# Kernel tuning notes

Measured on AMD Instinct MI355X. Metric: run time of the kernel, lower is better.

## Reference

```python
import jax, jax.numpy as jnp
import numpy as np

N, E, G, H, IN = 200000, 400000, 64, 128, 5
LN_EPS = 1e-5


def setup_inputs() -> dict:
    key = jax.random.key(0)
    ks = jax.random.split(key, 32)
    d = {}
    d["x"] = jax.random.normal(ks[0], (N, IN), jnp.float32)
    d["edge_index"] = jax.random.randint(ks[1], (2, E), 0, N, dtype=jnp.int32)
    d["edge_attr"] = jax.random.normal(ks[2], (E, 1), jnp.float32)
    d["batch"] = jnp.sort(jax.random.randint(ks[3], (N,), 0, G, dtype=jnp.int32))
    dims = [IN, H, H]
    i = 4
    names = [("ew", "eb", "w1_", "b1_", "w2_", "b2_", "g", "bt")]
    for l, din in enumerate(dims):
        d[f"ew{l}"] = jax.random.normal(ks[i], (1, din), jnp.float32); i += 1
        d[f"eb{l}"] = jnp.zeros((din,), jnp.float32)
        d[f"w1_{l}"] = jax.random.normal(ks[i], (din, H), jnp.float32) / np.sqrt(din); i += 1
        d[f"b1_{l}"] = jnp.zeros((H,), jnp.float32)
        d[f"w2_{l}"] = jax.random.normal(ks[i], (H, H), jnp.float32) / np.sqrt(H); i += 1
        d[f"b2_{l}"] = jnp.zeros((H,), jnp.float32)
        d[f"g{l}"] = jnp.ones((H,), jnp.float32)
        d[f"bt{l}"] = jnp.zeros((H,), jnp.float32)
    return d


def _gine_layer(x, src, dst, edge_attr, ew, eb, w1, b1, w2, b2, g, bt):
    # edge encoder: Linear(1, din)
    e = edge_attr @ ew + eb                       # [E, din]
    # GINEConv message: ReLU(x_j + e), aggregated (sum) at destination
    m = jax.nn.relu(x[src] + e)                   # [E, din]
    aggr = jax.ops.segment_sum(m, dst, num_segments=N)  # [N, din]
    h = x + aggr                                  # (1 + eps)*x with eps=0
    # GIN MLP: Linear -> ReLU -> Linear
    h = jax.nn.relu(h @ w1 + b1) @ w2 + b2        # [N, H]
    # LayerNorm
    mu = jnp.mean(h, axis=-1, keepdims=True)
    var = jnp.mean((h - mu) ** 2, axis=-1, keepdims=True)
    h = (h - mu) * jax.lax.rsqrt(var + LN_EPS) * g + bt
    return jax.nn.relu(h)


def reference(x, edge_index, edge_attr, batch,
              ew0, eb0, w1_0, b1_0, w2_0, b2_0, g0, bt0,
              ew1, eb1, w1_1, b1_1, w2_1, b2_1, g1, bt1,
              ew2, eb2, w1_2, b1_2, w2_2, b2_2, g2, bt2):
    src, dst = edge_index[0], edge_index[1]
    x = _gine_layer(x, src, dst, edge_attr, ew0, eb0, w1_0, b1_0, w2_0, b2_0, g0, bt0)
    x = _gine_layer(x, src, dst, edge_attr, ew1, eb1, w1_1, b1_1, w2_1, b2_1, g1, bt1)
    x = _gine_layer(x, src, dst, edge_attr, ew2, eb2, w1_2, b1_2, w2_2, b2_2, g2, bt2)
    # global pooling per graph
    add_pool = jax.ops.segment_sum(x, batch, num_segments=G)           # [G, H]
    counts = jax.ops.segment_sum(jnp.ones((N,), x.dtype), batch, num_segments=G)
    mean_pool = add_pool / jnp.maximum(counts, 1.0)[:, None]           # [G, H]
    return jnp.concatenate([mean_pool, add_pool], axis=1)              # [G, 2H]
```

## Files before the change

kernel.cpp:

```cpp
#include <hip/hip_runtime.h>

#define N_NODES 200000
#define N_EDGES 400000
#define N_GRAPHS 64
#define HDIM 128
#define INDIM 5
#define LN_EPS 1e-5f
#define LDA 138

typedef __attribute__((ext_vector_type(8))) short short8;
typedef __attribute__((ext_vector_type(4))) float f32x4;

__device__ __forceinline__ unsigned short to_bf(float v) {
    unsigned u = __builtin_bit_cast(unsigned, v);
    return (unsigned short)((u + 0x7FFFu + ((u >> 16) & 1u)) >> 16);
}
__device__ __forceinline__ float bf_lo(unsigned w) { return __builtin_bit_cast(float, w << 16); }
__device__ __forceinline__ float bf_hi(unsigned w) { return __builtin_bit_cast(float, w & 0xFFFF0000u); }
__device__ __forceinline__ float bf2f(unsigned short h) { return __builtin_bit_cast(float, (unsigned)h << 16); }


__global__ void hist_kernel(const int* __restrict__ ei, int* __restrict__ deg) {
    int e = blockIdx.x * blockDim.x + threadIdx.x;
    if (e < N_EDGES) atomicAdd(&deg[ei[N_EDGES + e]], 1);
}

#define SCAN_CHUNK 1024
#define SCAN_BLOCKS ((N_NODES + SCAN_CHUNK - 1) / SCAN_CHUNK)

__global__ __launch_bounds__(256) void scan_phaseA(const int* __restrict__ deg, int* __restrict__ bsums) {
    __shared__ int red[256];
    int t = threadIdx.x;
    int base = blockIdx.x * SCAN_CHUNK + t * 4;
    int s = 0;
#pragma unroll
    for (int k = 0; k < 4; ++k) {
        int i = base + k;
        s += (i < N_NODES) ? deg[i] : 0;
    }
    red[t] = s;
    __syncthreads();
    for (int off = 128; off; off >>= 1) {
        if (t < off) red[t] += red[t + off];
        __syncthreads();
    }
    if (t == 0) bsums[blockIdx.x] = red[0];
}

__global__ __launch_bounds__(256) void scan_phaseB(int* __restrict__ bsums, int* __restrict__ row_ptr) {
    __shared__ int s[256];
    int t = threadIdx.x;
    int v = (t < SCAN_BLOCKS) ? bsums[t] : 0;
    s[t] = v;
    __syncthreads();
    for (int off = 1; off < 256; off <<= 1) {
        int add = (t >= off) ? s[t - off] : 0;
        __syncthreads();
        s[t] += add;
        __syncthreads();
    }
    if (t < SCAN_BLOCKS) bsums[t] = s[t] - v;
    if (t == SCAN_BLOCKS - 1) row_ptr[N_NODES] = s[t];
}

__global__ __launch_bounds__(256) void scan_phaseC(const int* __restrict__ deg,
                                                   const int* __restrict__ bsums,
                                                   int* __restrict__ row_ptr) {
    __shared__ int ts[256];
    int t = threadIdx.x;
    int base = blockIdx.x * SCAN_CHUNK + t * 4;
    int v[4];
    int s = 0;
#pragma unroll
    for (int k = 0; k < 4; ++k) {
        int i = base + k;
        v[k] = (i < N_NODES) ? deg[i] : 0;
        s += v[k];
    }
    ts[t] = s;
    __syncthreads();
    for (int off = 1; off < 256; off <<= 1) {
        int add = (t >= off) ? ts[t - off] : 0;
        __syncthreads();
        ts[t] += add;
        __syncthreads();
    }
    int run = bsums[blockIdx.x] + ts[t] - s;
#pragma unroll
    for (int k = 0; k < 4; ++k) {
        int i = base + k;
        if (i < N_NODES) row_ptr[i] = run;
        run += v[k];
    }
}

__global__ void scatter_kernel(const int* __restrict__ ei, const float* __restrict__ ea,
                               const int* __restrict__ row_ptr, int* __restrict__ cursor,
                               int* __restrict__ csr_src, float* __restrict__ csr_val) {
    int e = blockIdx.x * blockDim.x + threadIdx.x;
    if (e >= N_EDGES) return;
    int d = ei[N_EDGES + e];
    int pos = atomicAdd(&cursor[d], 1);
    int slot = row_ptr[d] + pos;
    csr_src[slot] = ei[e];
    csr_val[slot] = ea[e];
}

__global__ void pack_w(const float* __restrict__ W, short* __restrict__ hi, int din, int KP) {
    int idx = blockIdx.x * 256 + threadIdx.x;
    if (idx >= KP * 128) return;
    int j = idx & 7;
    int lane = (idx >> 3) & 63;
    int rest = idx >> 9;
    int KS = KP >> 5;
    int kstep = rest % KS;
    int tile = rest / KS;
    int k = kstep * 32 + ((lane >> 4) * 8) + j;
    int n = tile * 16 + (lane & 15);
    float v = (k < din) ? W[k * 128 + n] : 0.f;
    hi[idx] = (short)to_bf(v);
}

template <int KP1, bool POOL>
__global__ __launch_bounds__(256, 4) void layer_fused(
    const void* __restrict__ xin_v, const int* __restrict__ row_ptr,
    const int* __restrict__ csr_src, const float* __restrict__ csr_val,
    const float* __restrict__ ew, const float* __restrict__ eb,
    const short* __restrict__ w1h, const float* __restrict__ b1,
    const short* __restrict__ w2h, const float* __restrict__ b2,
    const float* __restrict__ g, const float* __restrict__ bt,
    unsigned short* __restrict__ xout,
    const int* __restrict__ batch, float* __restrict__ pool, int* __restrict__ cnt) {
    __shared__ __align__(16) unsigned short A16[64 * LDA];
    __shared__ int bidx[64];
    union Scratch {
        float eweb[256];
        float part[64][4][INDIM];
    };
    __shared__ Scratch u;

    int tid = threadIdx.x;
    int node0 = blockIdx.x * 64;

    if (KP1 == 128) {
        const unsigned short* xin = (const unsigned short*)xin_v;
        if (tid < 32) ((float4*)u.eweb)[tid] = ((const float4*)ew)[tid];
        else if (tid < 64) ((float4*)u.eweb)[tid] = ((const float4*)eb)[tid - 32];
        if (POOL && tid >= 64 && tid < 128) bidx[tid - 64] = batch[node0 + tid - 64];

        int row = tid >> 2, qt = tid & 3, c0 = qt * 32;
        int node = node0 + row;
        float acc[32];
        {
            const uint4* xn = (const uint4*)(xin + (size_t)node * 128 + c0);
            uint4 uv[4];
#pragma unroll
            for (int j = 0; j < 4; ++j) uv[j] = xn[j];
            unsigned wds[16] = {uv[0].x, uv[0].y, uv[0].z, uv[0].w,
                                uv[1].x, uv[1].y, uv[1].z, uv[1].w,
                                uv[2].x, uv[2].y, uv[2].z, uv[2].w,
                                uv[3].x, uv[3].y, uv[3].z, uv[3].w};
#pragma unroll
            for (int i = 0; i < 16; ++i) {
                acc[2 * i] = bf_lo(wds[i]);
                acc[2 * i + 1] = bf_hi(wds[i]);
            }
        }
        int beg = row_ptr[node], end = row_ptr[node + 1];
        __syncthreads();

        for (int e = beg; e < end; ++e) {
            int s = csr_src[e];
            float a = csr_val[e];
            const uint4* xs = (const uint4*)(xin + (size_t)s * 128 + c0);
            uint4 uv[4];
#pragma unroll
            for (int j = 0; j < 4; ++j) uv[j] = xs[j];
            unsigned wds[16] = {uv[0].x, uv[0].y, uv[0].z, uv[0].w,
                                uv[1].x, uv[1].y, uv[1].z, uv[1].w,
                                uv[2].x, uv[2].y, uv[2].z, uv[2].w,
                                uv[3].x, uv[3].y, uv[3].z, uv[3].w};
#pragma unroll
            for (int i = 0; i < 16; ++i) {
                int cA = c0 + 2 * i, cB = cA + 1;
                acc[2 * i] += fmaxf(fmaf(a, u.eweb[cA], bf_lo(wds[i]) + u.eweb[128 + cA]), 0.f);
                acc[2 * i + 1] += fmaxf(fmaf(a, u.eweb[cB], bf_hi(wds[i]) + u.eweb[128 + cB]), 0.f);
            }
        }
        unsigned* Ar = (unsigned*)&A16[row * LDA + c0];
#pragma unroll
        for (int i = 0; i < 16; ++i)
            Ar[i] = (unsigned)to_bf(acc[2 * i]) | ((unsigned)to_bf(acc[2 * i + 1]) << 16);
    } else {
        const float* xinf = (const float*)xin_v;
        int row = tid >> 2, qt = tid & 3;
        int node = node0 + row;
        {
            float w[INDIM], b[INDIM], acc[INDIM];
#pragma unroll
            for (int j = 0; j < INDIM; ++j) {
                w[j] = ew[j];
                b[j] = eb[j];
                acc[j] = 0.f;
            }
            int beg = row_ptr[node], end = row_ptr[node + 1];
            for (int e = beg + qt; e < end; e += 4) {
                int s = csr_src[e];
                float a = csr_val[e];
#pragma unroll
                for (int j = 0; j < INDIM; ++j)
                    acc[j] += fmaxf(fmaf(a, w[j], xinf[s * INDIM + j] + b[j]), 0.f);
            }
#pragma unroll
            for (int j = 0; j < INDIM; ++j) u.part[row][qt][j] = acc[j];
        }
        __syncthreads();
        if (tid < 64) {
#pragma unroll
            for (int j = 0; j < INDIM; ++j) {
                float v = xinf[(node0 + tid) * INDIM + j] + u.part[tid][0][j] + u.part[tid][1][j] +
                          u.part[tid][2][j] + u.part[tid][3][j];
                A16[tid * LDA + j] = to_bf(v);
            }
#pragma unroll
            for (int j = INDIM; j < 32; ++j) A16[tid * LDA + j] = 0;
        }
        __syncthreads();
    }

    int wv = tid >> 6, lane = tid & 63;
    int mrow = lane & 15, q = lane >> 4;
    int arow = wv * 16 + mrow;

    const short8* w1p = (const short8*)w1h;
    const short8* w2p = (const short8*)w2h;

    f32x4 acc2[8];
#pragma unroll
    for (int t = 0; t < 8; ++t) acc2[t] = (f32x4){0.f, 0.f, 0.f, 0.f};
    constexpr int KS1 = KP1 / 32;
#pragma unroll
    for (int ks = 0; ks < KS1; ++ks) {
        short8 bh[8];
#pragma unroll
        for (int t = 0; t < 8; ++t) bh[t] = w1p[((size_t)t * KS1 + ks) * 64 + lane];
        short8 ah = *(const short8*)&A16[arow * LDA + ks * 32 + q * 8];
#pragma unroll
        for (int t = 0; t < 8; ++t)
            acc2[t] = __builtin_amdgcn_mfma_f32_16x16x32_bf16(ah, bh[t], acc2[t], 0, 0, 0);
    }
    {
        float b1v[8];
#pragma unroll
        for (int t = 0; t < 8; ++t) b1v[t] = b1[t * 16 + mrow];
#pragma unroll
        for (int t = 0; t < 8; ++t)
#pragma unroll
            for (int r = 0; r < 4; ++r) {
                int rrow = wv * 16 + q * 4 + r;
                int col = t * 16 + mrow;
                A16[rrow * LDA + col] = to_bf(fmaxf(acc2[t][r] + b1v[t], 0.f));
            }
    }

#pragma unroll
    for (int t = 0; t < 8; ++t) acc2[t] = (f32x4){0.f, 0.f, 0.f, 0.f};
#pragma unroll
    for (int ks = 0; ks < 4; ++ks) {
        short8 bh[8];
#pragma unroll
        for (int t = 0; t < 8; ++t) bh[t] = w2p[((size_t)t * 4 + ks) * 64 + lane];
        short8 ah = *(const short8*)&A16[arow * LDA + ks * 32 + q * 8];
#pragma unroll
        for (int t = 0; t < 8; ++t)
            acc2[t] = __builtin_amdgcn_mfma_f32_16x16x32_bf16(ah, bh[t], acc2[t], 0, 0, 0);
    }

    float s4[4] = {0.f, 0.f, 0.f, 0.f}, q4[4] = {0.f, 0.f, 0.f, 0.f};
    {
        float b2v[8];
#pragma unroll
        for (int t = 0; t < 8; ++t) b2v[t] = b2[t * 16 + mrow];
#pragma unroll
        for (int t = 0; t < 8; ++t)
#pragma unroll
            for (int r = 0; r < 4; ++r) {
                float v = acc2[t][r] + b2v[t];
                acc2[t][r] = v;
                s4[r] += v;
                q4[r] += v * v;
            }
    }
#pragma unroll
    for (int m = 1; m <= 8; m <<= 1) {
#pragma unroll
        for (int r = 0; r < 4; ++r) {
            s4[r] += __shfl_xor(s4[r], m, 64);
            q4[r] += __shfl_xor(q4[r], m, 64);
        }
    }
    float mu[4], inv[4];
#pragma unroll
    for (int r = 0; r < 4; ++r) {
        mu[r] = s4[r] * (1.f / HDIM);
        float var = q4[r] * (1.f / HDIM) - mu[r] * mu[r];
        inv[r] = rsqrtf(var + LN_EPS);
    }
    float gv[8], btv[8];
#pragma unroll
    for (int t = 0; t < 8; ++t) {
        gv[t] = g[t * 16 + mrow];
        btv[t] = bt[t * 16 + mrow];
    }

    __syncthreads();
#pragma unroll
    for (int t = 0; t < 8; ++t)
#pragma unroll
        for (int r = 0; r < 4; ++r) {
            int rrow = wv * 16 + q * 4 + r;
            int col = t * 16 + mrow;
            float o = fmaxf((acc2[t][r] - mu[r]) * inv[r] * gv[t] + btv[t], 0.f);
            A16[rrow * LDA + col] = to_bf(o);
        }
    __syncthreads();

    if (!POOL) {
        unsigned* xo = (unsigned*)xout;
#pragma unroll
        for (int i = 0; i < 16; ++i) {
            int idx = tid + 256 * i;
            int row = idx >> 6, w = idx & 63;
            xo[(size_t)(node0 + row) * 64 + w] = ((const unsigned*)&A16[row * LDA])[w];
        }
    } else {
        if (tid < 128) {
            int col = tid;
            float accp = 0.f;
            int cur = bidx[0];
            for (int r = 0; r < 64; ++r) {
                int gi = bidx[r];
                if (gi != cur) {
                    unsafeAtomicAdd(&pool[cur * HDIM + col], accp);
                    accp = 0.f;
                    cur = gi;
                }
                accp += bf2f(A16[r * LDA + col]);
            }
            unsafeAtomicAdd(&pool[cur * HDIM + col], accp);
        } else if (tid == 255) {
            int cur = bidx[0], c = 0;
            for (int r = 0; r < 64; ++r) {
                if (bidx[r] != cur) {
                    atomicAdd(&cnt[cur], c);
                    c = 0;
                    cur = bidx[r];
                }
                ++c;
            }
            atomicAdd(&cnt[cur], c);
        }
    }
}

__global__ void pool_final(const float* __restrict__ pool, const int* __restrict__ cnt,
                           float* __restrict__ out) {
    int g = blockIdx.x, j = threadIdx.x;
    float add = pool[g * HDIM + j];
    float c = (float)max(cnt[g], 1);
    out[g * (2 * HDIM) + j] = add / c;
    out[g * (2 * HDIM) + HDIM + j] = add;
}

extern "C" void kernel_launch(void* const* d_in, const int* in_sizes, int n_in,
                              void* d_out, int out_size, void* d_ws, size_t ws_size,
                              hipStream_t stream) {
    const float* x_in = (const float*)d_in[0];
    const int* ei = (const int*)d_in[1];
    const float* ea = (const float*)d_in[2];
    const int* batch = (const int*)d_in[3];
    const float* P[24];
    for (int i = 0; i < 24; ++i) P[i] = (const float*)d_in[4 + i];

    unsigned short* x_a = (unsigned short*)d_ws;
    unsigned short* x_b = x_a + (size_t)N_NODES * HDIM;
    float* pool = (float*)(x_b + (size_t)N_NODES * HDIM);
    int* cnt = (int*)(pool + N_GRAPHS * HDIM);
    int* deg = cnt + N_GRAPHS;
    int* cursor = deg + N_NODES;
    int* row_ptr = cursor + N_NODES;
    int* bsums = row_ptr + N_NODES + 1;
    int* csr_src = bsums + 256;
    float* csr_val = (float*)(csr_src + N_EDGES);
    short* wp = (short*)(((uintptr_t)(csr_val + N_EDGES) + 15) & ~(uintptr_t)15);
    float* out = (float*)d_out;

    short *w1h[3], *w2h[3];
    for (int l = 0; l < 3; ++l) {
        w1h[l] = wp + (size_t)l * 32768;
        w2h[l] = w1h[l] + 16384;
    }

    hipMemsetAsync(pool, 0,
                   (N_GRAPHS * HDIM + N_GRAPHS + 2 * N_NODES) * sizeof(int), stream);

    hist_kernel<<<(N_EDGES + 255) / 256, 256, 0, stream>>>(ei, deg);
    scan_phaseA<<<SCAN_BLOCKS, 256, 0, stream>>>(deg, bsums);
    scan_phaseB<<<1, 256, 0, stream>>>(bsums, row_ptr);
    scan_phaseC<<<SCAN_BLOCKS, 256, 0, stream>>>(deg, bsums, row_ptr);
    scatter_kernel<<<(N_EDGES + 255) / 256, 256, 0, stream>>>(ei, ea, row_ptr, cursor, csr_src, csr_val);

    pack_w<<<16, 256, 0, stream>>>(P[2], w1h[0], INDIM, 32);
    pack_w<<<64, 256, 0, stream>>>(P[4], w2h[0], 128, 128);
    for (int l = 1; l < 3; ++l) {
        pack_w<<<64, 256, 0, stream>>>(P[8 * l + 2], w1h[l], 128, 128);
        pack_w<<<64, 256, 0, stream>>>(P[8 * l + 4], w2h[l], 128, 128);
    }

    layer_fused<32, false><<<N_NODES / 64, 256, 0, stream>>>(
        x_in, row_ptr, csr_src, csr_val, P[0], P[1],
        w1h[0], P[3], w2h[0], P[5], P[6], P[7], x_a, nullptr, nullptr, nullptr);
    layer_fused<128, false><<<N_NODES / 64, 256, 0, stream>>>(
        x_a, row_ptr, csr_src, csr_val, P[8], P[9],
        w1h[1], P[11], w2h[1], P[13], P[14], P[15], x_b, nullptr, nullptr, nullptr);
    layer_fused<128, true><<<N_NODES / 64, 256, 0, stream>>>(
        x_b, row_ptr, csr_src, csr_val, P[16], P[17],
        w1h[2], P[19], w2h[2], P[21], P[22], P[23], nullptr, batch, pool, cnt);

    pool_final<<<N_GRAPHS, HDIM, 0, stream>>>(pool, cnt, out);
}
```

Measured before the change: 368.2 us.

## Interleave CSR src/value, unroll edge gather by two, merge weight packing launches

Stores CSR source index and edge value together as an int2 so each edge needs one load. Unrolls the per-node neighbour gather loop by two so two rows' loads are in flight at once. Merges six weight-packing launches into one kernel and changes the LDS row stride from 138 to 136. Also removes a __syncthreads before the LayerNorm write-back into shared memory, which risks a race if other waves are still reading A16.

```diff
diff --git a/kernel.cpp b/kernel.cpp
--- a/kernel.cpp
+++ b/kernel.cpp
@@ -6,7 +6,7 @@
 #define HDIM 128
 #define INDIM 5
 #define LN_EPS 1e-5f
-#define LDA 138
+#define LDA 136
 
 typedef __attribute__((ext_vector_type(8))) short short8;
 typedef __attribute__((ext_vector_type(4))) float f32x4;
@@ -96,18 +96,31 @@
 
 __global__ void scatter_kernel(const int* __restrict__ ei, const float* __restrict__ ea,
                                const int* __restrict__ row_ptr, int* __restrict__ cursor,
-                               int* __restrict__ csr_src, float* __restrict__ csr_val) {
+                               int2* __restrict__ csr) {
     int e = blockIdx.x * blockDim.x + threadIdx.x;
     if (e >= N_EDGES) return;
     int d = ei[N_EDGES + e];
     int pos = atomicAdd(&cursor[d], 1);
-    int slot = row_ptr[d] + pos;
-    csr_src[slot] = ei[e];
-    csr_val[slot] = ea[e];
-}
-
-__global__ void pack_w(const float* __restrict__ W, short* __restrict__ hi, int din, int KP) {
-    int idx = blockIdx.x * 256 + threadIdx.x;
+    csr[row_ptr[d] + pos] = make_int2(ei[e], __float_as_int(ea[e]));
+}
+
+__global__ void pack_all(const float* __restrict__ s0, short* __restrict__ d0,
+                         const float* __restrict__ s1, short* __restrict__ d1,
+                         const float* __restrict__ s2, short* __restrict__ d2,
+                         const float* __restrict__ s3, short* __restrict__ d3,
+                         const float* __restrict__ s4, short* __restrict__ d4,
+                         const float* __restrict__ s5, short* __restrict__ d5) {
+    int b = blockIdx.x;
+    const float* W;
+    short* D;
+    int din, KP, b0;
+    if (b < 16)       { W = s0; D = d0; din = 5;   KP = 32;  b0 = 0; }
+    else if (b < 80)  { W = s1; D = d1; din = 128; KP = 128; b0 = 16; }
+    else if (b < 144) { W = s2; D = d2; din = 128; KP = 128; b0 = 80; }
+    else if (b < 208) { W = s3; D = d3; din = 128; KP = 128; b0 = 144; }
+    else if (b < 272) { W = s4; D = d4; din = 128; KP = 128; b0 = 208; }
+    else              { W = s5; D = d5; din = 128; KP = 128; b0 = 272; }
+    int idx = (b - b0) * 256 + threadIdx.x;
     if (idx >= KP * 128) return;
     int j = idx & 7;
     int lane = (idx >> 3) & 63;
@@ -118,13 +131,13 @@
     int k = kstep * 32 + ((lane >> 4) * 8) + j;
     int n = tile * 16 + (lane & 15);
     float v = (k < din) ? W[k * 128 + n] : 0.f;
-    hi[idx] = (short)to_bf(v);
+    D[idx] = (short)to_bf(v);
 }
 
 template <int KP1, bool POOL>
 __global__ __launch_bounds__(256, 4) void layer_fused(
     const void* __restrict__ xin_v, const int* __restrict__ row_ptr,
-    const int* __restrict__ csr_src, const float* __restrict__ csr_val,
+    const int2* __restrict__ csr,
     const float* __restrict__ ew, const float* __restrict__ eb,
     const short* __restrict__ w1h, const float* __restrict__ b1,
     const short* __restrict__ w2h, const float* __restrict__ b2,
@@ -169,22 +182,44 @@
         int beg = row_ptr[node], end = row_ptr[node + 1];
         __syncthreads();
 
-        for (int e = beg; e < end; ++e) {
-            int s = csr_src[e];
-            float a = csr_val[e];
-            const uint4* xs = (const uint4*)(xin + (size_t)s * 128 + c0);
-            uint4 uv[4];
-#pragma unroll
-            for (int j = 0; j < 4; ++j) uv[j] = xs[j];
-            unsigned wds[16] = {uv[0].x, uv[0].y, uv[0].z, uv[0].w,
-                                uv[1].x, uv[1].y, uv[1].z, uv[1].w,
-                                uv[2].x, uv[2].y, uv[2].z, uv[2].w,
-                                uv[3].x, uv[3].y, uv[3].z, uv[3].w};
+        int e = beg;
+        for (; e + 2 <= end; e += 2) {
+            int2 r0 = csr[e], r1 = csr[e + 1];
+            float a0 = __int_as_float(r0.y), a1 = __int_as_float(r1.y);
+            const uint4* p0 = (const uint4*)(xin + (size_t)r0.x * 128 + c0);
+            const uint4* p1 = (const uint4*)(xin + (size_t)r1.x * 128 + c0);
+            uint4 u0[4], u1[4];
+#pragma unroll
+            for (int j = 0; j < 4; ++j) { u0[j] = p0[j]; u1[j] = p1[j]; }
+            unsigned w0[16] = {u0[0].x, u0[0].y, u0[0].z, u0[0].w, u0[1].x, u0[1].y, u0[1].z, u0[1].w,
+                               u0[2].x, u0[2].y, u0[2].z, u0[2].w, u0[3].x, u0[3].y, u0[3].z, u0[3].w};
+            unsigned w1v[16] = {u1[0].x, u1[0].y, u1[0].z, u1[0].w, u1[1].x, u1[1].y, u1[1].z, u1[1].w,
+                                u1[2].x, u1[2].y, u1[2].z, u1[2].w, u1[3].x, u1[3].y, u1[3].z, u1[3].w};
 #pragma unroll
             for (int i = 0; i < 16; ++i) {
                 int cA = c0 + 2 * i, cB = cA + 1;
-                acc[2 * i] += fmaxf(fmaf(a, u.eweb[cA], bf_lo(wds[i]) + u.eweb[128 + cA]), 0.f);
-                acc[2 * i + 1] += fmaxf(fmaf(a, u.eweb[cB], bf_hi(wds[i]) + u.eweb[128 + cB]), 0.f);
+                float ewA = u.eweb[cA], ewB = u.eweb[cB];
+                float ebA = u.eweb[128 + cA], ebB = u.eweb[128 + cB];
+                acc[2 * i]     += fmaxf(fmaf(a0, ewA, bf_lo(w0[i]) + ebA), 0.f)
+                                + fmaxf(fmaf(a1, ewA, bf_lo(w1v[i]) + ebA), 0.f);
+                acc[2 * i + 1] += fmaxf(fmaf(a0, ewB, bf_hi(w0[i]) + ebB), 0.f)
+                                + fmaxf(fmaf(a1, ewB, bf_hi(w1v[i]) + ebB), 0.f);
+            }
+        }
+        if (e < end) {
+            int2 r0 = csr[e];
+            float a0 = __int_as_float(r0.y);
+            const uint4* p0 = (const uint4*)(xin + (size_t)r0.x * 128 + c0);
+            uint4 u0[4];
+#pragma unroll
+            for (int j = 0; j < 4; ++j) u0[j] = p0[j];
+            unsigned w0[16] = {u0[0].x, u0[0].y, u0[0].z, u0[0].w, u0[1].x, u0[1].y, u0[1].z, u0[1].w,
+                               u0[2].x, u0[2].y, u0[2].z, u0[2].w, u0[3].x, u0[3].y, u0[3].z, u0[3].w};
+#pragma unroll
+            for (int i = 0; i < 16; ++i) {
+                int cA = c0 + 2 * i, cB = cA + 1;
+                acc[2 * i]     += fmaxf(fmaf(a0, u.eweb[cA], bf_lo(w0[i]) + u.eweb[128 + cA]), 0.f);
+                acc[2 * i + 1] += fmaxf(fmaf(a0, u.eweb[cB], bf_hi(w0[i]) + u.eweb[128 + cB]), 0.f);
             }
         }
         unsigned* Ar = (unsigned*)&A16[row * LDA + c0];
@@ -205,11 +240,11 @@
             }
             int beg = row_ptr[node], end = row_ptr[node + 1];
             for (int e = beg + qt; e < end; e += 4) {
-                int s = csr_src[e];
-                float a = csr_val[e];
+                int2 r = csr[e];
+                float a = __int_as_float(r.y);
 #pragma unroll
                 for (int j = 0; j < INDIM; ++j)
-                    acc[j] += fmaxf(fmaf(a, w[j], xinf[s * INDIM + j] + b[j]), 0.f);
+                    acc[j] += fmaxf(fmaf(a, w[j], xinf[r.x * INDIM + j] + b[j]), 0.f);
             }
 #pragma unroll
             for (int j = 0; j < INDIM; ++j) u.part[row][qt][j] = acc[j];
@@ -313,7 +348,6 @@
         btv[t] = bt[t * 16 + mrow];
     }
 
-    __syncthreads();
 #pragma unroll
     for (int t = 0; t < 8; ++t)
 #pragma unroll
@@ -390,9 +424,8 @@
     int* cursor = deg + N_NODES;
     int* row_ptr = cursor + N_NODES;
     int* bsums = row_ptr + N_NODES + 1;
-    int* csr_src = bsums + 256;
-    float* csr_val = (float*)(csr_src + N_EDGES);
-    short* wp = (short*)(((uintptr_t)(csr_val + N_EDGES) + 15) & ~(uintptr_t)15);
+    int2* csr = (int2*)(bsums + 256);
+    short* wp = (short*)(((uintptr_t)(csr + N_EDGES) + 15) & ~(uintptr_t)15);
     float* out = (float*)d_out;
 
     short *w1h[3], *w2h[3];
@@ -408,23 +441,20 @@
     scan_phaseA<<<SCAN_BLOCKS, 256, 0, stream>>>(deg, bsums);
     scan_phaseB<<<1, 256, 0, stream>>>(bsums, row_ptr);
     scan_phaseC<<<SCAN_BLOCKS, 256, 0, stream>>>(deg, bsums, row_ptr);
-    scatter_kernel<<<(N_EDGES + 255) / 256, 256, 0, stream>>>(ei, ea, row_ptr, cursor, csr_src, csr_val);
-
-    pack_w<<<16, 256, 0, stream>>>(P[2], w1h[0], INDIM, 32);
-    pack_w<<<64, 256, 0, stream>>>(P[4], w2h[0], 128, 128);
-    for (int l = 1; l < 3; ++l) {
-        pack_w<<<64, 256, 0, stream>>>(P[8 * l + 2], w1h[l], 128, 128);
-        pack_w<<<64, 256, 0, stream>>>(P[8 * l + 4], w2h[l], 128, 128);
-    }
+    scatter_kernel<<<(N_EDGES + 255) / 256, 256, 0, stream>>>(ei, ea, row_ptr, cursor, csr);
+
+    pack_all<<<336, 256, 0, stream>>>(P[2], w1h[0], P[4], w2h[0],
+                                      P[10], w1h[1], P[12], w2h[1],
+                                      P[18], w1h[2], P[20], w2h[2]);
 
     layer_fused<32, false><<<N_NODES / 64, 256, 0, stream>>>(
-        x_in, row_ptr, csr_src, csr_val, P[0], P[1],
+        x_in, row_ptr, csr, P[0], P[1],
         w1h[0], P[3], w2h[0], P[5], P[6], P[7], x_a, nullptr, nullptr, nullptr);
     layer_fused<128, false><<<N_NODES / 64, 256, 0, stream>>>(
-        x_a, row_ptr, csr_src, csr_val, P[8], P[9],
+        x_a, row_ptr, csr, P[8], P[9],
         w1h[1], P[11], w2h[1], P[13], P[14], P[15], x_b, nullptr, nullptr, nullptr);
     layer_fused<128, true><<<N_NODES / 64, 256, 0, stream>>>(
-        x_b, row_ptr, csr_src, csr_val, P[16], P[17],
+        x_b, row_ptr, csr, P[16], P[17],
         w1h[2], P[19], w2h[2], P[21], P[22], P[23], nullptr, batch, pool, cnt);
 
     pool_final<<<N_GRAPHS, HDIM, 0, stream>>>(pool, cnt, out);
```

Measured after the change: 395.5 us. 7.4% more time.
